# Kernel tuning notes

Measured on AMD Instinct MI355X. Metric: run time of the kernel, lower is better.

The kernel has to match this reference:

```python
import jax, jax.numpy as jnp
import numpy as np

B, C, H, W = 8, 3, 512, 512
EPS = 2e-4
N_ITER = 10  # n_iter_max default in TvChambolleDenoiser.forward


def setup_inputs() -> dict:
    key = jax.random.key(0)
    k1, k2 = jax.random.split(key)
    image = jax.random.normal(k1, (B, C, H, W), dtype=jnp.float32)
    # per-image denoising strength, typical TV weights
    weight = jax.random.uniform(k2, (B,), dtype=jnp.float32, minval=0.05, maxval=0.15)
    return {"image": image, "weight": weight}


def _denoise_tv_2d(img, w, eps=EPS, n_iter=N_ITER):
    """Chambolle TV denoising of a single 2D image (faithful to the torch loop)."""
    tau = 0.25  # 1 / (2 * ndim), ndim = 2
    numel = img.shape[0] * img.shape[1]

    def body(carry, i):
        pt, out, E_init, E_prev, done = carry
        # divergence of dual variable pt: dt = -pt.sum(0); dt[1:,:] += pt[0,:-1,:]; dt[:,1:] += pt[1,:,:-1]
        dt = -(pt[0] + pt[1])
        dt = dt.at[1:, :].add(pt[0, :-1, :])
        dt = dt.at[:, 1:].add(pt[1, :, :-1])
        out_new = jnp.where(i > 0, img + dt, img)
        Et = jnp.where(i > 0, jnp.sum(dt * dt), jnp.float32(0.0))
        # forward finite differences, zero-padded at the far boundary (gt stays 0 there)
        g0 = jnp.pad(out_new[1:, :] - out_new[:-1, :], ((0, 1), (0, 0)))
        g1 = jnp.pad(out_new[:, 1:] - out_new[:, :-1], ((0, 0), (0, 1)))
        s = g0 * g0 + g1 * g1
        # safe sqrt (forward value identical; avoids NaN grads at exact zeros)
        norm = jnp.sqrt(jnp.where(s > 0, s, 1.0)) * (s > 0)
        Et = (Et + w * jnp.sum(norm)) / numel
        gt = jnp.stack([g0, g1])  # [2, H, W]
        pt_new = (pt - tau * gt) / (1.0 + (tau / w) * norm)[None]
        E_init_new = jnp.where(i == 0, Et, E_init)
        converged = (i > 0) & (jnp.abs(E_prev - Et) < eps * E_init_new)
        # once converged (break in the torch loop), freeze all state
        pt = jnp.where(done, pt, pt_new)
        out = jnp.where(done, out, out_new)
        E_prev = jnp.where(done, E_prev, Et)
        E_init = jnp.where(done, E_init, E_init_new)
        done = done | converged
        return (pt, out, E_init, E_prev, done), None

    carry0 = (
        jnp.zeros((2,) + img.shape, img.dtype),  # pt
        img,                                      # out
        jnp.float32(0.0),                         # E_init
        jnp.float32(0.0),                         # E_previous
        jnp.bool_(False),                         # done
    )
    (pt, out, E_init, E_prev, done), _ = jax.lax.scan(body, carry0, jnp.arange(n_iter))
    return out


def reference(image, weight):
    b, c, h, w = image.shape
    imgs = image.reshape(b * c, h, w)          # each (batch, channel) slice denoised independently
    ws = jnp.repeat(weight, c)                 # per-batch weight shared across channels
    out = jax.vmap(_denoise_tv_2d)(imgs, ws)
    return out.reshape(b, c, h, w)
```

## Files before the change

kernel.cpp:

```cpp
#include <hip/hip_runtime.h>
#include <hip/hip_fp16.h>
#include <math.h>
#include <stdint.h>

#define HH 512
#define WW 512
#define NIMG 24
#define CCH 3
#define TAU 0.25f
#define TVEPS 2e-4f
#define NUMEL 262144.0f

#define TSO 60
#define NT 9

#define LSF 69
#define LSH 70


__device__ __forceinline__ float2 h2f(uint32_t v) {
    __half2 h; *reinterpret_cast<uint32_t*>(&h) = v;
    return __half22float2(h);
}
__device__ __forceinline__ uint32_t f2h2(float a, float b) {
    __half2 h = __floats2half2_rn(a, b);
    return *reinterpret_cast<uint32_t*>(&h);
}
__device__ __forceinline__ void h4_to_f(uint2 hv, float* f) {
    float2 a = h2f(hv.x), b = h2f(hv.y);
    f[0] = a.x; f[1] = a.y; f[2] = b.x; f[3] = b.y;
}

__device__ __forceinline__ int SUMIX(int slot, int arr, int im) {
    return ((slot * 4 + arr) * NIMG + im) * 96;
}

__device__ __forceinline__ void red4_store(float a, float b, float c, float d,
                                           float* pa, float* pb, float* pc, float* pdd,
                                           int tid) {
    for (int off = 32; off > 0; off >>= 1) {
        a += __shfl_down(a, off, 64);
        b += __shfl_down(b, off, 64);
        c += __shfl_down(c, off, 64);
        d += __shfl_down(d, off, 64);
    }
    __shared__ float sr[4][4];
    int wave = tid >> 6, lane = tid & 63;
    if (lane == 0) { sr[0][wave] = a; sr[1][wave] = b; sr[2][wave] = c; sr[3][wave] = d; }
    __syncthreads();
    if (tid == 0) {
        *pa = (sr[0][0] + sr[0][1]) + (sr[0][2] + sr[0][3]);
        *pb = (sr[1][0] + sr[1][1]) + (sr[1][2] + sr[1][3]);
        *pc = (sr[2][0] + sr[2][1]) + (sr[2][2] + sr[2][3]);
        *pdd = (sr[3][0] + sr[3][1]) + (sr[3][2] + sr[3][3]);
    }
}

struct Smem {
    uint32_t PT[68 * LSF];
    float    OA[68 * LSF];
    __half   IM[68 * LSH];
};

__device__ void stage_pt_im(Smem& S, const uint32_t* __restrict__ ptg,
                            const __half* __restrict__ hI,
                            int x0, int y0, int tid) {
    for (int idx = tid; idx < 68 * 34; idx += 256) {
        int r = idx / 34, mq = idx - r * 34;
        int c = 2 * mq;
        int y = y0 - 2 + r, x = x0 - 2 + c;
        uint2 pv = make_uint2(0u, 0u);
        uint32_t iv = 0u;
        if ((unsigned)y < (unsigned)HH && (unsigned)x < (unsigned)WW) {
            size_t off = (size_t)y * WW + x;
            pv = *(const uint2*)(ptg + off);
            iv = *(const uint32_t*)(hI + off);
        }
        S.PT[r * LSF + c] = pv.x;
        S.PT[r * LSF + c + 1] = pv.y;
        *(uint32_t*)&S.IM[r * LSH + c] = iv;
    }
}

__device__ void phase_outA_x(Smem& S, int tid) {
    for (int idx = tid; idx < 67 * 67; idx += 256) {
        int r = idx / 67, c = idx - r * 67;
        r += 1; c += 1;
        float2 cf = h2f(S.PT[r * LSF + c]);
        float up = h2f(S.PT[(r - 1) * LSF + c]).x;
        float lf = h2f(S.PT[r * LSF + c - 1]).y;
        float im = __half2float(S.IM[r * LSH + c]);
        S.OA[r * LSF + c] = im + (-(cf.x + cf.y) + up + lf);
    }
}

__device__ void phase_ptA_x(Smem& S, int x0, int y0, int tid, float tw) {
    for (int idx = tid; idx < 66 * 66; idx += 256) {
        int r = idx / 66, c = idx - r * 66;
        r += 1; c += 1;
        int y = y0 - 2 + r, x = x0 - 2 + c;
        if ((unsigned)y < (unsigned)HH && (unsigned)x < (unsigned)WW) {
            float o = S.OA[r * LSF + c];
            float g0 = (y < HH - 1) ? S.OA[(r + 1) * LSF + c] - o : 0.f;
            float g1 = (x < WW - 1) ? S.OA[r * LSF + c + 1] - o : 0.f;
            float ss2 = g0 * g0 + g1 * g1;
            float nrm = (ss2 > 0.f) ? sqrtf(ss2) : 0.f;
            float inv = __builtin_amdgcn_rcpf(1.f + tw * nrm);
            float2 cf = h2f(S.PT[r * LSF + c]);
            S.PT[r * LSF + c] = f2h2((cf.x - TAU * g0) * inv, (cf.y - TAU * g1) * inv);
        } else {
            S.PT[r * LSF + c] = 0u;
        }
    }
}

__global__ __launch_bounds__(256, 4) void tv_step0(
    const float* __restrict__ img, const float* __restrict__ weight,
    __half* __restrict__ imgh, uint32_t* __restrict__ ptout,
    float* __restrict__ pn0)
{
    const int im = blockIdx.z;
    const int bid = blockIdx.y * 8 + blockIdx.x;
    const float w = weight[im / CCH];
    const int x0 = blockIdx.x * 64, y0 = blockIdx.y * 64;
    const float* imgI = img + (size_t)im * HH * WW;
    __half* hI = imgh + (size_t)im * HH * WW;
    uint32_t* pI = ptout + (size_t)im * HH * WW;
    __shared__ float s[65][68];
    const int tid = threadIdx.x;
    const int tx = tid & 15, ry = tid >> 4;
    const int gx = x0 + 4 * tx;

    float o[4][4];
    #pragma unroll
    for (int i = 0; i < 4; ++i) {
        int ey = ry + 16 * i, gy = y0 + ey;
        float4 v = *(const float4*)(imgI + (size_t)gy * WW + gx);
        o[i][0] = v.x; o[i][1] = v.y; o[i][2] = v.z; o[i][3] = v.w;
        *(float4*)&s[ey][4 * tx] = v;
    }
    if (tx == 15 && x0 + 64 < WW) {
        #pragma unroll
        for (int i = 0; i < 4; ++i) {
            int ey = ry + 16 * i, gy = y0 + ey;
            s[ey][64] = imgI[(size_t)gy * WW + x0 + 64];
        }
    }
    if (ry == 0 && y0 + 64 < HH) {
        *(float4*)&s[64][4 * tx] = *(const float4*)(imgI + (size_t)(y0 + 64) * WW + gx);
    }
    __syncthreads();

    float accn = 0.f;
    const float tw = TAU / w;
    #pragma unroll
    for (int i = 0; i < 4; ++i) {
        int ey = ry + 16 * i, gy = y0 + ey;
        float4 dn = *(float4*)&s[ey + 1][4 * tx];
        float rt_sh = __shfl_down(o[i][0], 1, 64);
        float rt = (tx == 15) ? s[ey][64] : rt_sh;
        float dnv[4] = {dn.x, dn.y, dn.z, dn.w};
        uint32_t pv[4];
        #pragma unroll
        for (int j = 0; j < 4; ++j) {
            float ov = o[i][j];
            float g0 = (gy < HH - 1) ? dnv[j] - ov : 0.f;
            float rn = (j < 3) ? o[i][j + 1] : rt;
            float g1 = (gx + j < WW - 1) ? rn - ov : 0.f;
            float ss2 = g0 * g0 + g1 * g1;
            float nrm = (ss2 > 0.f) ? sqrtf(ss2) : 0.f;
            accn += nrm;
            float inv = __builtin_amdgcn_rcpf(1.f + tw * nrm);
            pv[j] = f2h2(-TAU * g0 * inv, -TAU * g1 * inv);
        }
        size_t off = (size_t)gy * WW + gx;
        *(uint4*)(pI + off) = make_uint4(pv[0], pv[1], pv[2], pv[3]);
        *(uint2*)(hI + off) = make_uint2(f2h2(o[i][0], o[i][1]), f2h2(o[i][2], o[i][3]));
    }
    for (int off = 32; off > 0; off >>= 1) accn += __shfl_down(accn, off, 64);
    __shared__ float sr[4];
    if ((tid & 63) == 0) sr[tid >> 6] = accn;
    __syncthreads();
    if (tid == 0) pn0[im * 96 + bid] = (sr[0] + sr[1]) + (sr[2] + sr[3]);
}

__global__ __launch_bounds__(256, 3) void tv_fused(
    int m,
    const __half* __restrict__ imgh, const float* __restrict__ weight,
    const uint32_t* __restrict__ pt_in, uint32_t* __restrict__ pt_out,
    float* __restrict__ sc, float* __restrict__ sums)
{
    const int im = blockIdx.z;
    const int bx = blockIdx.x, by = blockIdx.y;
    const int bid = by * NT + bx;
    const int tid = threadIdx.x;
    const float w = weight[im / CCH];

    __shared__ int sh_done;
    __shared__ float hsum[2][4];
    {
        const int sIn = (m - 1) & 1;
        float da = 0.f, na = 0.f, db = 0.f, nb = 0.f;
        if (m == 1) {
            if (tid < 64) na = sums[SUMIX(0, 1, im) + tid];
        } else if (tid < 81) {
            da = sums[SUMIX(sIn, 0, im) + tid];
            na = sums[SUMIX(sIn, 1, im) + tid];
            db = sums[SUMIX(sIn, 2, im) + tid];
            nb = sums[SUMIX(sIn, 3, im) + tid];
        }
        if (tid < 128) {
            for (int off = 32; off > 0; off >>= 1) {
                da += __shfl_down(da, off, 64);
                na += __shfl_down(na, off, 64);
                db += __shfl_down(db, off, 64);
                nb += __shfl_down(nb, off, 64);
            }
            if ((tid & 63) == 0) {
                hsum[tid >> 6][0] = da; hsum[tid >> 6][1] = na;
                hsum[tid >> 6][2] = db; hsum[tid >> 6][3] = nb;
            }
        }
        __syncthreads();
        if (tid == 0) {
            float tda = hsum[0][0] + hsum[1][0];
            float tna = hsum[0][1] + hsum[1][1];
            float tdb = hsum[0][2] + hsum[1][2];
            float tnb = hsum[0][3] + hsum[1][3];
            float Eprev, Einit; int done, lastk;
            if (m == 1) {
                float E0 = w * tna / NUMEL;
                Eprev = E0; Einit = E0; done = 0; lastk = 0;
            } else {
                const float* sI = sc + ((m - 1) & 1) * 128;
                Eprev = sI[im]; Einit = sI[32 + im];
                done = ((const int*)sI)[64 + im];
                lastk = ((const int*)sI)[96 + im];
                if (!done) {
                    float Et = (tda + w * tna) / NUMEL;
                    if (fabsf(Eprev - Et) < TVEPS * Einit) { done = 1; lastk = 2 * m - 3; }
                    else {
                        Eprev = Et;
                        Et = (tdb + w * tnb) / NUMEL;
                        if (fabsf(Eprev - Et) < TVEPS * Einit) { done = 1; lastk = 2 * m - 2; }
                        else Eprev = Et;
                    }
                }
            }
            if (bid == 0) {
                float* sO = sc + (m & 1) * 128;
                sO[im] = Eprev; sO[32 + im] = Einit;
                ((int*)sO)[64 + im] = done;
                ((int*)sO)[96 + im] = lastk;
            }
            sh_done = done;
        }
    }
    __syncthreads();
    if (sh_done) return;

    const float tw = TAU / w;
    const uint32_t* pinI = pt_in + (size_t)im * HH * WW;
    uint32_t* poutI = pt_out + (size_t)im * HH * WW;
    const __half* hI = imgh + (size_t)im * HH * WW;

    const int tx = tid & 15, ty = tid >> 4;
    const int wx0 = TSO * bx - 2, wy0 = TSO * by - 2;
    const int cx0 = wx0 + 4 * tx;
    const int ry0 = wy0 + 4 * ty;

    __shared__ uint4  XP[16][16];
    __shared__ float4 XO[16][16];

    uint32_t c[4][4];
    uint32_t ihp[4][2];
    const bool interior = (wx0 >= 0) && (wx0 + 64 <= WW) && (wy0 >= 0) && (wy0 + 64 <= HH);
    if (interior) {
        #pragma unroll
        for (int i = 0; i < 4; ++i) {
            size_t off = (size_t)(ry0 + i) * WW + cx0;
            uint2 a = *(const uint2*)(pinI + off);
            uint2 b = *(const uint2*)(pinI + off + 2);
            c[i][0] = a.x; c[i][1] = a.y; c[i][2] = b.x; c[i][3] = b.y;
            ihp[i][0] = *(const uint32_t*)(hI + off);
            ihp[i][1] = *(const uint32_t*)(hI + off + 2);
        }
    } else {
        #pragma unroll
        for (int i = 0; i < 4; ++i) {
            int gy = ry0 + i;
            unsigned short us[4];
            #pragma unroll
            for (int j = 0; j < 4; ++j) {
                int gxj = cx0 + j;
                bool in = ((unsigned)gy < (unsigned)HH) && ((unsigned)gxj < (unsigned)WW);
                c[i][j] = in ? pinI[(size_t)gy * WW + gxj] : 0u;
                us[j] = in ? *(const unsigned short*)(hI + (size_t)gy * WW + gxj)
                           : (unsigned short)0;
            }
            ihp[i][0] = (uint32_t)us[0] | ((uint32_t)us[1] << 16);
            ihp[i][1] = (uint32_t)us[2] | ((uint32_t)us[3] << 16);
        }
    }
    XP[ty][tx] = make_uint4(c[3][0], c[3][1], c[3][2], c[3][3]);
    __syncthreads();

    float o[4][4];
    float accda = 0.f;
    {
        uint4 up4 = (ty > 0) ? XP[ty - 1][tx] : make_uint4(0u, 0u, 0u, 0u);
        uint32_t ua[4] = {up4.x, up4.y, up4.z, up4.w};
        #pragma unroll
        for (int i = 0; i < 4; ++i) {
            uint32_t lw = __shfl_up(c[i][3], 1, 64);
            int gy = ry0 + i;
            bool r_ok = (unsigned)(4 * ty + i - 2) < 60u && gy < HH;
            #pragma unroll
            for (int j = 0; j < 4; ++j) {
                float2 cf = h2f(c[i][j]);
                float up = (i > 0) ? h2f(c[i - 1][j]).x : h2f(ua[j]).x;
                float le = (j > 0) ? h2f(c[i][j - 1]).y : h2f(lw).y;
                float dv = -(cf.x + cf.y) + up + le;
                float2 i2 = h2f(ihp[i][j >> 1]);
                float imv = (j & 1) ? i2.y : i2.x;
                o[i][j] = imv + dv;
                bool own = r_ok && ((unsigned)(4 * tx + j - 2) < 60u) && (cx0 + j < WW);
                accda += own ? dv * dv : 0.f;
            }
        }
    }

    uint32_t pa[4][4];
    float accna = 0.f;
    XO[ty][tx] = make_float4(o[0][0], o[0][1], o[0][2], o[0][3]);
    __syncthreads();
    {
        float4 b4 = (ty < 15) ? XO[ty + 1][tx] : make_float4(0.f, 0.f, 0.f, 0.f);
        float bel[4] = {b4.x, b4.y, b4.z, b4.w};
        #pragma unroll
        for (int i = 0; i < 4; ++i) {
            float rsh = __shfl_down(o[i][0], 1, 64);
            int gy = ry0 + i;
            bool r_ok = (unsigned)(4 * ty + i - 2) < 60u && gy < HH;
            #pragma unroll
            for (int j = 0; j < 4; ++j) {
                int gxj = cx0 + j;
                float ov = o[i][j];
                float below = (i < 3) ? o[i + 1][j] : bel[j];
                float right = (j < 3) ? o[i][j + 1] : rsh;
                float g0 = (gy < HH - 1) ? below - ov : 0.f;
                float g1 = (gxj < WW - 1) ? right - ov : 0.f;
                float ss2 = g0 * g0 + g1 * g1;
                float nrm = (ss2 > 0.f) ? sqrtf(ss2) : 0.f;
                float inv = __builtin_amdgcn_rcpf(1.f + tw * nrm);
                float2 cf = h2f(c[i][j]);
                uint32_t pvv = f2h2((cf.x - TAU * g0) * inv, (cf.y - TAU * g1) * inv);
                bool vp = ((unsigned)gy < (unsigned)HH) && ((unsigned)gxj < (unsigned)WW);
                pa[i][j] = vp ? pvv : 0u;
                bool own = r_ok && ((unsigned)(4 * tx + j - 2) < 60u) && (gxj < WW);
                accna += own ? nrm : 0.f;
            }
        }
    }

    float ob[4][4];
    float accdb = 0.f;
    XP[ty][tx] = make_uint4(pa[3][0], pa[3][1], pa[3][2], pa[3][3]);
    __syncthreads();
    {
        uint4 up4 = (ty > 0) ? XP[ty - 1][tx] : make_uint4(0u, 0u, 0u, 0u);
        uint32_t ua[4] = {up4.x, up4.y, up4.z, up4.w};
        #pragma unroll
        for (int i = 0; i < 4; ++i) {
            uint32_t lw = __shfl_up(pa[i][3], 1, 64);
            int gy = ry0 + i;
            bool r_ok = (unsigned)(4 * ty + i - 2) < 60u && gy < HH;
            #pragma unroll
            for (int j = 0; j < 4; ++j) {
                float2 cf = h2f(pa[i][j]);
                float up = (i > 0) ? h2f(pa[i - 1][j]).x : h2f(ua[j]).x;
                float le = (j > 0) ? h2f(pa[i][j - 1]).y : h2f(lw).y;
                float dv = -(cf.x + cf.y) + up + le;
                float2 i2 = h2f(ihp[i][j >> 1]);
                float imv = (j & 1) ? i2.y : i2.x;
                ob[i][j] = imv + dv;
                bool own = r_ok && ((unsigned)(4 * tx + j - 2) < 60u) && (cx0 + j < WW);
                accdb += own ? dv * dv : 0.f;
            }
        }
    }

    float accnb = 0.f;
    XO[ty][tx] = make_float4(ob[0][0], ob[0][1], ob[0][2], ob[0][3]);
    __syncthreads();
    {
        float4 b4 = (ty < 15) ? XO[ty + 1][tx] : make_float4(0.f, 0.f, 0.f, 0.f);
        float bel[4] = {b4.x, b4.y, b4.z, b4.w};
        #pragma unroll
        for (int i = 0; i < 4; ++i) {
            float rsh = __shfl_down(ob[i][0], 1, 64);
            int gy = ry0 + i;
            bool r_ok = ((unsigned)(4 * ty + i - 2) < 60u) && (gy < HH);
            uint32_t pv[4];
            #pragma unroll
            for (int j = 0; j < 4; ++j) {
                int gxj = cx0 + j;
                float ov = ob[i][j];
                float below = (i < 3) ? ob[i + 1][j] : bel[j];
                float right = (j < 3) ? ob[i][j + 1] : rsh;
                float g0 = (gy < HH - 1) ? below - ov : 0.f;
                float g1 = (gxj < WW - 1) ? right - ov : 0.f;
                float ss2 = g0 * g0 + g1 * g1;
                float nrm = (ss2 > 0.f) ? sqrtf(ss2) : 0.f;
                float inv = __builtin_amdgcn_rcpf(1.f + tw * nrm);
                float2 cf = h2f(pa[i][j]);
                uint32_t pvv = f2h2((cf.x - TAU * g0) * inv, (cf.y - TAU * g1) * inv);
                bool vp = ((unsigned)gy < (unsigned)HH) && ((unsigned)gxj < (unsigned)WW);
                pv[j] = vp ? pvv : 0u;
                bool own = r_ok && ((unsigned)(4 * tx + j - 2) < 60u) && (gxj < WW);
                accnb += own ? nrm : 0.f;
            }
            if (r_ok) {
                size_t off = (size_t)gy * WW + cx0;
                if (tx > 0 && cx0 < WW)
                    *(uint2*)(poutI + off) = make_uint2(pv[0], pv[1]);
                if (tx < 15 && cx0 + 2 < WW)
                    *(uint2*)(poutI + off + 2) = make_uint2(pv[2], pv[3]);
            }
        }
    }

    const int sOut = m & 1;
    red4_store(accda, accna, accdb, accnb,
               &sums[SUMIX(sOut, 0, im) + bid], &sums[SUMIX(sOut, 1, im) + bid],
               &sums[SUMIX(sOut, 2, im) + bid], &sums[SUMIX(sOut, 3, im) + bid], tid);
}

__global__ __launch_bounds__(256, 3) void tv_out(
    const float* __restrict__ img, float* __restrict__ out,
    const uint32_t* __restrict__ ptA, const uint32_t* __restrict__ ptB,
    const __half* __restrict__ imgh, const float* __restrict__ weight,
    const float* __restrict__ sc, const float* __restrict__ sums)
{
    const int im = blockIdx.z;
    const int tid = threadIdx.x;
    const float w = weight[im / CCH];

    __shared__ int2 shk;
    __shared__ float hsum[2][4];
    {
        const float* sI = sc;
        int done = ((const int*)sI)[64 + im];
        int lastk = ((const int*)sI)[96 + im];
        float da = 0.f, na = 0.f, db = 0.f, nb = 0.f;
        if (!done && tid < 81) {
            da = sums[SUMIX(0, 0, im) + tid];
            na = sums[SUMIX(0, 1, im) + tid];
            db = sums[SUMIX(0, 2, im) + tid];
            nb = sums[SUMIX(0, 3, im) + tid];
        }
        if (tid < 128) {
            for (int off = 32; off > 0; off >>= 1) {
                da += __shfl_down(da, off, 64);
                na += __shfl_down(na, off, 64);
                db += __shfl_down(db, off, 64);
                nb += __shfl_down(nb, off, 64);
            }
            if ((tid & 63) == 0) {
                hsum[tid >> 6][0] = da; hsum[tid >> 6][1] = na;
                hsum[tid >> 6][2] = db; hsum[tid >> 6][3] = nb;
            }
        }
        __syncthreads();
        if (tid == 0) {
            if (!done) {
                float tda = hsum[0][0] + hsum[1][0];
                float tna = hsum[0][1] + hsum[1][1];
                float tdb = hsum[0][2] + hsum[1][2];
                float tnb = hsum[0][3] + hsum[1][3];
                float Eprev = sI[im], Einit = sI[32 + im];
                float Et = (tda + w * tna) / NUMEL;
                if (fabsf(Eprev - Et) < TVEPS * Einit) { done = 1; lastk = 7; }
                else {
                    Eprev = Et;
                    Et = (tdb + w * tnb) / NUMEL;
                    if (fabsf(Eprev - Et) < TVEPS * Einit) { done = 1; lastk = 8; }
                }
            }
            shk.x = done; shk.y = lastk;
        }
    }
    __syncthreads();
    const int k = shk.x ? shk.y : 9;

    const float* imgI = img + (size_t)im * HH * WW;
    float* outI = out + (size_t)im * HH * WW;
    const int x0 = blockIdx.x * 64, y0 = blockIdx.y * 64;
    const int tx = tid & 15, ry = tid >> 4;
    const int gx = x0 + 4 * tx;

    if (k & 1) {
        const uint32_t* p = ((((k - 1) >> 1) & 1) ? ptB : ptA) + (size_t)im * HH * WW;
        #pragma unroll
        for (int i = 0; i < 4; ++i) {
            int gy = y0 + ry + 16 * i;
            size_t off = (size_t)gy * WW + gx;
            uint4 cv = *(const uint4*)(p + off);
            uint4 uv = make_uint4(0u, 0u, 0u, 0u);
            if (gy > 0) uv = *(const uint4*)(p + off - WW);
            uint32_t lf = (gx > 0) ? p[off - 1] : 0u;
            float4 iv = *(const float4*)(imgI + off);
            uint32_t cc[4] = {cv.x, cv.y, cv.z, cv.w};
            uint32_t uu[4] = {uv.x, uv.y, uv.z, uv.w};
            uint32_t lt[4] = {lf, cv.x, cv.y, cv.z};
            float ivv[4] = {iv.x, iv.y, iv.z, iv.w};
            float r[4];
            #pragma unroll
            for (int j = 0; j < 4; ++j) {
                float2 cf = h2f(cc[j]);
                r[j] = ivv[j] + (-(cf.x + cf.y) + h2f(uu[j]).x + h2f(lt[j]).y);
            }
            *(float4*)(outI + off) = make_float4(r[0], r[1], r[2], r[3]);
        }
    } else {
        const uint32_t* p = ((((k - 2) >> 1) & 1) ? ptB : ptA) + (size_t)im * HH * WW;
        const __half* hI = imgh + (size_t)im * HH * WW;
        const float tw = TAU / w;
        __shared__ Smem S;
        stage_pt_im(S, p, hI, x0, y0, tid);
        __syncthreads();
        phase_outA_x(S, tid);
        __syncthreads();
        phase_ptA_x(S, x0, y0, tid, tw);
        __syncthreads();
        #pragma unroll
        for (int i = 0; i < 4; ++i) {
            int gy = y0 + ry + 16 * i;
            int r = 2 + ry + 16 * i;
            size_t off = (size_t)gy * WW + gx;
            float4 iv = *(const float4*)(imgI + off);
            float ivv[4] = {iv.x, iv.y, iv.z, iv.w};
            float rr[4];
            #pragma unroll
            for (int j = 0; j < 4; ++j) {
                int cix = 2 + 4 * tx + j;
                float2 cf = h2f(S.PT[r * LSF + cix]);
                float up = h2f(S.PT[(r - 1) * LSF + cix]).x;
                float lf = h2f(S.PT[r * LSF + cix - 1]).y;
                rr[j] = ivv[j] + (-(cf.x + cf.y) + up + lf);
            }
            *(float4*)(outI + off) = make_float4(rr[0], rr[1], rr[2], rr[3]);
        }
    }
}

extern "C" void kernel_launch(void* const* d_in, const int* in_sizes, int n_in,
                              void* d_out, int out_size, void* d_ws, size_t ws_size,
                              hipStream_t stream)
{
    const float* img = (const float*)d_in[0];
    const float* weight = (const float*)d_in[1];
    float* out = (float*)d_out;
    float* sc = (float*)d_ws;
    float* sums = (float*)((char*)d_ws + 4096);
    __half* imgh = (__half*)((char*)d_ws + 131072);
    uint32_t* ptA = (uint32_t*)((char*)d_ws + 12713984);
    uint32_t* ptB = (uint32_t*)((char*)d_ws + 37879808);

    dim3 block(256);

    float* pn0 = sums + 1 * NIMG * 96;
    tv_step0<<<dim3(8, 8, NIMG), block, 0, stream>>>(img, weight, imgh, ptA, pn0);

    for (int m = 1; m <= 4; ++m) {
        uint32_t* pin  = (m & 1) ? ptA : ptB;
        uint32_t* pout = (m & 1) ? ptB : ptA;
        tv_fused<<<dim3(NT, NT, NIMG), block, 0, stream>>>(m, imgh, weight, pin, pout, sc, sums);
    }

    tv_out<<<dim3(8, 8, NIMG), block, 0, stream>>>(img, out, ptA, ptB, imgh, weight, sc, sums);
}
```

Measured before the change: 231.8 us.

## Make each wavefront own an independent 32x32 tile, replacing LDS exchange with shuffles

Each 256-thread block now holds four independent wavefront tiles of 32x32 (28x28 owned plus halo) instead of one 64x64 block tile. The vertical neighbor exchange goes through __shfl_up/down by 8 lanes instead of shared memory, which removes the four __syncthreads and the LDS arrays. The convergence preamble is also reduced per wavefront, so no block barrier is needed. In exchange the halo fraction rises (28/32 vs 60/64 owned), so more redundant loads and compute, and the grid becomes 10x10 tiles with 100 partial sums per image.

```diff
diff --git a/kernel.cpp b/kernel.cpp
--- a/kernel.cpp
+++ b/kernel.cpp
@@ -11,8 +11,7 @@
 #define TVEPS 2e-4f
 #define NUMEL 262144.0f
 
-#define TSO 60
-#define NT 9
+#define NTB 10
 
 #define LSF 69
 #define LSH 70
@@ -26,13 +25,9 @@
     __half2 h = __floats2half2_rn(a, b);
     return *reinterpret_cast<uint32_t*>(&h);
 }
-__device__ __forceinline__ void h4_to_f(uint2 hv, float* f) {
-    float2 a = h2f(hv.x), b = h2f(hv.y);
-    f[0] = a.x; f[1] = a.y; f[2] = b.x; f[3] = b.y;
-}
 
 __device__ __forceinline__ int SUMIX(int slot, int arr, int im) {
-    return ((slot * 4 + arr) * NIMG + im) * 96;
+    return ((slot * 4 + arr) * NIMG + im) * 128;
 }
 
 __device__ __forceinline__ void red4_store(float a, float b, float c, float d,
@@ -181,7 +176,7 @@
     __shared__ float sr[4];
     if ((tid & 63) == 0) sr[tid >> 6] = accn;
     __syncthreads();
-    if (tid == 0) pn0[im * 96 + bid] = (sr[0] + sr[1]) + (sr[2] + sr[3]);
+    if (tid == 0) pn0[im * 128 + bid] = (sr[0] + sr[1]) + (sr[2] + sr[3]);
 }
 
 __global__ __launch_bounds__(256, 3) void tv_fused(
@@ -192,89 +187,81 @@
 {
     const int im = blockIdx.z;
     const int bx = blockIdx.x, by = blockIdx.y;
-    const int bid = by * NT + bx;
+    const int bid = by * NTB + bx;
     const int tid = threadIdx.x;
+    const int lane = tid & 63, wid = tid >> 6;
     const float w = weight[im / CCH];
 
-    __shared__ int sh_done;
-    __shared__ float hsum[2][4];
+    int done, lastk;
+    float Eprev, Einit;
     {
         const int sIn = (m - 1) & 1;
         float da = 0.f, na = 0.f, db = 0.f, nb = 0.f;
         if (m == 1) {
-            if (tid < 64) na = sums[SUMIX(0, 1, im) + tid];
-        } else if (tid < 81) {
-            da = sums[SUMIX(sIn, 0, im) + tid];
-            na = sums[SUMIX(sIn, 1, im) + tid];
-            db = sums[SUMIX(sIn, 2, im) + tid];
-            nb = sums[SUMIX(sIn, 3, im) + tid];
-        }
-        if (tid < 128) {
-            for (int off = 32; off > 0; off >>= 1) {
-                da += __shfl_down(da, off, 64);
-                na += __shfl_down(na, off, 64);
-                db += __shfl_down(db, off, 64);
-                nb += __shfl_down(nb, off, 64);
-            }
-            if ((tid & 63) == 0) {
-                hsum[tid >> 6][0] = da; hsum[tid >> 6][1] = na;
-                hsum[tid >> 6][2] = db; hsum[tid >> 6][3] = nb;
-            }
-        }
-        __syncthreads();
-        if (tid == 0) {
-            float tda = hsum[0][0] + hsum[1][0];
-            float tna = hsum[0][1] + hsum[1][1];
-            float tdb = hsum[0][2] + hsum[1][2];
-            float tnb = hsum[0][3] + hsum[1][3];
-            float Eprev, Einit; int done, lastk;
-            if (m == 1) {
-                float E0 = w * tna / NUMEL;
-                Eprev = E0; Einit = E0; done = 0; lastk = 0;
-            } else {
-                const float* sI = sc + ((m - 1) & 1) * 128;
-                Eprev = sI[im]; Einit = sI[32 + im];
-                done = ((const int*)sI)[64 + im];
-                lastk = ((const int*)sI)[96 + im];
-                if (!done) {
-                    float Et = (tda + w * tna) / NUMEL;
-                    if (fabsf(Eprev - Et) < TVEPS * Einit) { done = 1; lastk = 2 * m - 3; }
-                    else {
-                        Eprev = Et;
-                        Et = (tdb + w * tnb) / NUMEL;
-                        if (fabsf(Eprev - Et) < TVEPS * Einit) { done = 1; lastk = 2 * m - 2; }
-                        else Eprev = Et;
-                    }
+            na = sums[SUMIX(0, 1, im) + lane];
+        } else {
+            da = sums[SUMIX(sIn, 0, im) + lane];
+            na = sums[SUMIX(sIn, 1, im) + lane];
+            db = sums[SUMIX(sIn, 2, im) + lane];
+            nb = sums[SUMIX(sIn, 3, im) + lane];
+            if (lane < 36) {
+                da += sums[SUMIX(sIn, 0, im) + 64 + lane];
+                na += sums[SUMIX(sIn, 1, im) + 64 + lane];
+                db += sums[SUMIX(sIn, 2, im) + 64 + lane];
+                nb += sums[SUMIX(sIn, 3, im) + 64 + lane];
+            }
+        }
+        for (int off = 32; off > 0; off >>= 1) {
+            da += __shfl_down(da, off, 64);
+            na += __shfl_down(na, off, 64);
+            db += __shfl_down(db, off, 64);
+            nb += __shfl_down(nb, off, 64);
+        }
+        float tda = __shfl(da, 0, 64), tna = __shfl(na, 0, 64);
+        float tdb = __shfl(db, 0, 64), tnb = __shfl(nb, 0, 64);
+        if (m == 1) {
+            float E0 = w * tna / NUMEL;
+            Eprev = E0; Einit = E0; done = 0; lastk = 0;
+        } else {
+            const float* sI = sc + ((m - 1) & 1) * 128;
+            Eprev = sI[im]; Einit = sI[32 + im];
+            done = ((const int*)sI)[64 + im];
+            lastk = ((const int*)sI)[96 + im];
+            if (!done) {
+                float Et = (tda + w * tna) / NUMEL;
+                if (fabsf(Eprev - Et) < TVEPS * Einit) { done = 1; lastk = 2 * m - 3; }
+                else {
+                    Eprev = Et;
+                    Et = (tdb + w * tnb) / NUMEL;
+                    if (fabsf(Eprev - Et) < TVEPS * Einit) { done = 1; lastk = 2 * m - 2; }
+                    else Eprev = Et;
                 }
             }
-            if (bid == 0) {
-                float* sO = sc + (m & 1) * 128;
-                sO[im] = Eprev; sO[32 + im] = Einit;
-                ((int*)sO)[64 + im] = done;
-                ((int*)sO)[96 + im] = lastk;
-            }
-            sh_done = done;
-        }
-    }
-    __syncthreads();
-    if (sh_done) return;
+        }
+        if (bid == 0 && tid == 0) {
+            float* sO = sc + (m & 1) * 128;
+            sO[im] = Eprev; sO[32 + im] = Einit;
+            ((int*)sO)[64 + im] = done;
+            ((int*)sO)[96 + im] = lastk;
+        }
+    }
+    if (done) return;
 
     const float tw = TAU / w;
     const uint32_t* pinI = pt_in + (size_t)im * HH * WW;
     uint32_t* poutI = pt_out + (size_t)im * HH * WW;
     const __half* hI = imgh + (size_t)im * HH * WW;
 
-    const int tx = tid & 15, ty = tid >> 4;
-    const int wx0 = TSO * bx - 2, wy0 = TSO * by - 2;
-    const int cx0 = wx0 + 4 * tx;
-    const int ry0 = wy0 + 4 * ty;
-
-    __shared__ uint4  XP[16][16];
-    __shared__ float4 XO[16][16];
+    const int wxq = wid & 1, wyq = wid >> 1;
+    const int lx = lane & 7, ly = lane >> 3;
+    const int ox0 = 56 * bx + 28 * wxq;
+    const int oy0 = 56 * by + 28 * wyq;
+    const int cx0 = ox0 - 2 + 4 * lx;
+    const int ry0 = oy0 - 2 + 4 * ly;
 
     uint32_t c[4][4];
     uint32_t ihp[4][2];
-    const bool interior = (wx0 >= 0) && (wx0 + 64 <= WW) && (wy0 >= 0) && (wy0 + 64 <= HH);
+    const bool interior = (ox0 >= 2) && (ox0 + 30 <= WW) && (oy0 >= 2) && (oy0 + 30 <= HH);
     if (interior) {
         #pragma unroll
         for (int i = 0; i < 4; ++i) {
@@ -302,19 +289,18 @@
             ihp[i][1] = (uint32_t)us[2] | ((uint32_t)us[3] << 16);
         }
     }
-    XP[ty][tx] = make_uint4(c[3][0], c[3][1], c[3][2], c[3][3]);
-    __syncthreads();
 
     float o[4][4];
     float accda = 0.f;
     {
-        uint4 up4 = (ty > 0) ? XP[ty - 1][tx] : make_uint4(0u, 0u, 0u, 0u);
-        uint32_t ua[4] = {up4.x, up4.y, up4.z, up4.w};
+        uint32_t ua[4];
+        #pragma unroll
+        for (int j = 0; j < 4; ++j) ua[j] = __shfl_up(c[3][j], 8, 64);
         #pragma unroll
         for (int i = 0; i < 4; ++i) {
             uint32_t lw = __shfl_up(c[i][3], 1, 64);
             int gy = ry0 + i;
-            bool r_ok = (unsigned)(4 * ty + i - 2) < 60u && gy < HH;
+            bool r_ok = ((unsigned)(4 * ly + i - 2) < 28u) && (gy < HH);
             #pragma unroll
             for (int j = 0; j < 4; ++j) {
                 float2 cf = h2f(c[i][j]);
@@ -324,7 +310,7 @@
                 float2 i2 = h2f(ihp[i][j >> 1]);
                 float imv = (j & 1) ? i2.y : i2.x;
                 o[i][j] = imv + dv;
-                bool own = r_ok && ((unsigned)(4 * tx + j - 2) < 60u) && (cx0 + j < WW);
+                bool own = r_ok && ((unsigned)(4 * lx + j - 2) < 28u) && (cx0 + j < WW);
                 accda += own ? dv * dv : 0.f;
             }
         }
@@ -332,16 +318,15 @@
 
     uint32_t pa[4][4];
     float accna = 0.f;
-    XO[ty][tx] = make_float4(o[0][0], o[0][1], o[0][2], o[0][3]);
-    __syncthreads();
     {
-        float4 b4 = (ty < 15) ? XO[ty + 1][tx] : make_float4(0.f, 0.f, 0.f, 0.f);
-        float bel[4] = {b4.x, b4.y, b4.z, b4.w};
+        float bel[4];
+        #pragma unroll
+        for (int j = 0; j < 4; ++j) bel[j] = __shfl_down(o[0][j], 8, 64);
         #pragma unroll
         for (int i = 0; i < 4; ++i) {
             float rsh = __shfl_down(o[i][0], 1, 64);
             int gy = ry0 + i;
-            bool r_ok = (unsigned)(4 * ty + i - 2) < 60u && gy < HH;
+            bool r_ok = ((unsigned)(4 * ly + i - 2) < 28u) && (gy < HH);
             #pragma unroll
             for (int j = 0; j < 4; ++j) {
                 int gxj = cx0 + j;
@@ -357,7 +342,7 @@
                 uint32_t pvv = f2h2((cf.x - TAU * g0) * inv, (cf.y - TAU * g1) * inv);
                 bool vp = ((unsigned)gy < (unsigned)HH) && ((unsigned)gxj < (unsigned)WW);
                 pa[i][j] = vp ? pvv : 0u;
-                bool own = r_ok && ((unsigned)(4 * tx + j - 2) < 60u) && (gxj < WW);
+                bool own = r_ok && ((unsigned)(4 * lx + j - 2) < 28u) && (gxj < WW);
                 accna += own ? nrm : 0.f;
             }
         }
@@ -365,16 +350,15 @@
 
     float ob[4][4];
     float accdb = 0.f;
-    XP[ty][tx] = make_uint4(pa[3][0], pa[3][1], pa[3][2], pa[3][3]);
-    __syncthreads();
     {
-        uint4 up4 = (ty > 0) ? XP[ty - 1][tx] : make_uint4(0u, 0u, 0u, 0u);
-        uint32_t ua[4] = {up4.x, up4.y, up4.z, up4.w};
+        uint32_t ua[4];
+        #pragma unroll
+        for (int j = 0; j < 4; ++j) ua[j] = __shfl_up(pa[3][j], 8, 64);
         #pragma unroll
         for (int i = 0; i < 4; ++i) {
             uint32_t lw = __shfl_up(pa[i][3], 1, 64);
             int gy = ry0 + i;
-            bool r_ok = (unsigned)(4 * ty + i - 2) < 60u && gy < HH;
+            bool r_ok = ((unsigned)(4 * ly + i - 2) < 28u) && (gy < HH);
             #pragma unroll
             for (int j = 0; j < 4; ++j) {
                 float2 cf = h2f(pa[i][j]);
@@ -384,23 +368,22 @@
                 float2 i2 = h2f(ihp[i][j >> 1]);
                 float imv = (j & 1) ? i2.y : i2.x;
                 ob[i][j] = imv + dv;
-                bool own = r_ok && ((unsigned)(4 * tx + j - 2) < 60u) && (cx0 + j < WW);
+                bool own = r_ok && ((unsigned)(4 * lx + j - 2) < 28u) && (cx0 + j < WW);
                 accdb += own ? dv * dv : 0.f;
             }
         }
     }
 
     float accnb = 0.f;
-    XO[ty][tx] = make_float4(ob[0][0], ob[0][1], ob[0][2], ob[0][3]);
-    __syncthreads();
     {
-        float4 b4 = (ty < 15) ? XO[ty + 1][tx] : make_float4(0.f, 0.f, 0.f, 0.f);
-        float bel[4] = {b4.x, b4.y, b4.z, b4.w};
+        float bel[4];
+        #pragma unroll
+        for (int j = 0; j < 4; ++j) bel[j] = __shfl_down(ob[0][j], 8, 64);
         #pragma unroll
         for (int i = 0; i < 4; ++i) {
             float rsh = __shfl_down(ob[i][0], 1, 64);
             int gy = ry0 + i;
-            bool r_ok = ((unsigned)(4 * ty + i - 2) < 60u) && (gy < HH);
+            bool r_ok = ((unsigned)(4 * ly + i - 2) < 28u) && (gy < HH);
             uint32_t pv[4];
             #pragma unroll
             for (int j = 0; j < 4; ++j) {
@@ -417,14 +400,14 @@
                 uint32_t pvv = f2h2((cf.x - TAU * g0) * inv, (cf.y - TAU * g1) * inv);
                 bool vp = ((unsigned)gy < (unsigned)HH) && ((unsigned)gxj < (unsigned)WW);
                 pv[j] = vp ? pvv : 0u;
-                bool own = r_ok && ((unsigned)(4 * tx + j - 2) < 60u) && (gxj < WW);
+                bool own = r_ok && ((unsigned)(4 * lx + j - 2) < 28u) && (gxj < WW);
                 accnb += own ? nrm : 0.f;
             }
             if (r_ok) {
                 size_t off = (size_t)gy * WW + cx0;
-                if (tx > 0 && cx0 < WW)
+                if (lx > 0 && cx0 < WW)
                     *(uint2*)(poutI + off) = make_uint2(pv[0], pv[1]);
-                if (tx < 15 && cx0 + 2 < WW)
+                if (lx < 7 && cx0 + 2 < WW)
                     *(uint2*)(poutI + off + 2) = make_uint2(pv[2], pv[3]);
             }
         }
@@ -453,7 +436,7 @@
         int done = ((const int*)sI)[64 + im];
         int lastk = ((const int*)sI)[96 + im];
         float da = 0.f, na = 0.f, db = 0.f, nb = 0.f;
-        if (!done && tid < 81) {
+        if (!done && tid < 100) {
             da = sums[SUMIX(0, 0, im) + tid];
             na = sums[SUMIX(0, 1, im) + tid];
             db = sums[SUMIX(0, 2, im) + tid];
@@ -569,13 +552,13 @@
 
     dim3 block(256);
 
-    float* pn0 = sums + 1 * NIMG * 96;
+    float* pn0 = sums + 1 * NIMG * 128;
     tv_step0<<<dim3(8, 8, NIMG), block, 0, stream>>>(img, weight, imgh, ptA, pn0);
 
     for (int m = 1; m <= 4; ++m) {
         uint32_t* pin  = (m & 1) ? ptA : ptB;
         uint32_t* pout = (m & 1) ? ptB : ptA;
-        tv_fused<<<dim3(NT, NT, NIMG), block, 0, stream>>>(m, imgh, weight, pin, pout, sc, sums);
+        tv_fused<<<dim3(NTB, NTB, NIMG), block, 0, stream>>>(m, imgh, weight, pin, pout, sc, sums);
     }
 
     tv_out<<<dim3(8, 8, NIMG), block, 0, stream>>>(img, out, ptA, ptB, imgh, weight, sc, sums);
```

Measured after the change: 225.3 us. -2.8%, faster.
